# Performance work log

Hardware: AMD Instinct MI355X
Metric: run time of the kernel (lower is better)

The kernel has to match this reference:

```python
import jax, jax.numpy as jnp
import numpy as np

N, H, W, C = 128, 256, 256, 3
P = 1.0
XFLIP = 1.0
YFLIP = 1.0
ROTATE_INT = 1.0
TRANSLATE_INT = 1.0
TRANSLATE_INT_MAX = 0.125


def setup_inputs() -> dict:
    key = jax.random.key(0)
    ks = jax.random.split(key, 9)
    return {
        'images': jax.random.normal(ks[0], (N, H, W, C), dtype=jnp.float32),
        'xflip_w': jax.random.randint(ks[1], (N, 1, 1, 1), 0, 2, dtype=jnp.int32),
        'xflip_gate': jax.random.uniform(ks[2], (N, 1, 1, 1), dtype=jnp.float32),
        'yflip_w': jax.random.randint(ks[3], (N, 1, 1, 1), 0, 2, dtype=jnp.int32),
        'yflip_gate': jax.random.uniform(ks[4], (N, 1, 1, 1), dtype=jnp.float32),
        'rot_w': jax.random.randint(ks[5], (N, 1, 1, 1), 0, 4, dtype=jnp.int32),
        'rot_gate': jax.random.uniform(ks[6], (N, 1, 1, 1), dtype=jnp.float32),
        'trans_w': jax.random.uniform(ks[7], (2, N, 1, 1, 1), dtype=jnp.float32),
        'trans_gate': jax.random.uniform(ks[8], (1, N, 1, 1, 1), dtype=jnp.float32),
    }


def _augment(images, xflip_w, xflip_gate, yflip_w, yflip_gate, rot_w, rot_gate,
             trans_w, trans_gate):
    n, h, w_, c = images.shape

    # --- x-flip (per-sample gated horizontal flip) ---
    wv = jnp.where(xflip_gate < XFLIP * P, xflip_w, jnp.zeros_like(xflip_w))
    images = jnp.where(wv == 1, jnp.flip(images, 2), images)

    # --- y-flip ---
    wv = jnp.where(yflip_gate < YFLIP * P, yflip_w, jnp.zeros_like(yflip_w))
    images = jnp.where(wv == 1, jnp.flip(images, 1), images)

    # --- 90-degree rotations (requires H == W) ---
    wv = jnp.where(rot_gate < ROTATE_INT * P, rot_w, jnp.zeros_like(rot_w))
    images = jnp.where((wv == 1) | (wv == 2), jnp.flip(images, 2), images)
    images = jnp.where((wv == 2) | (wv == 3), jnp.flip(images, 1), images)
    images = jnp.where((wv == 1) | (wv == 3), jnp.transpose(images, (0, 2, 1, 3)), images)

    # --- integer translation with reflection padding (gather) ---
    tw = trans_w * 2.0 - 1.0                                   # [2,N,1,1,1] in [-1,1)
    tw = jnp.where(trans_gate < TRANSLATE_INT * P, tw, jnp.zeros_like(tw))
    tx = jnp.round(tw[0] * w_ * TRANSLATE_INT_MAX).astype(jnp.int32)[:, 0, 0, 0]  # [N]
    ty = jnp.round(tw[1] * h * TRANSLATE_INT_MAX).astype(jnp.int32)[:, 0, 0, 0]   # [N]
    tx = jax.lax.stop_gradient(tx)
    ty = jax.lax.stop_gradient(ty)
    # reflected source indices per sample: [N, W] and [N, H]
    xi = w_ - 1 - jnp.abs(w_ - 1 - (jnp.arange(w_)[None, :] - tx[:, None]) % (w_ * 2 - 2))
    yi = h - 1 - jnp.abs(h - 1 - (jnp.arange(h)[None, :] + ty[:, None]) % (h * 2 - 2))
    images = jax.vmap(lambda im, y, x: im[y][:, x])(images, yi, xi)
    return images


def reference(images, xflip_w, xflip_gate, yflip_w, yflip_gate, rot_w, rot_gate,
              trans_w, trans_gate):
    return _augment(images, xflip_w, xflip_gate, yflip_w, yflip_gate,
                    rot_w, rot_gate, trans_w, trans_gate)
```

## Files before the change

### kernel.cpp

```cpp
#include <hip/hip_runtime.h>

#define NN 128
#define HH 256
#define WW 256
#define CC 3
#define HWC (HH * WW * CC)
#define TILE 32
#define LSTRIDE 100
#define ROWF (WW * CC)

__device__ __forceinline__ int reflect_idx(int v, int size) {
    int period = 2 * size - 2;
    int m = v % period;
    if (m < 0) m += period;
    return size - 1 - abs(size - 1 - m);
}

__global__ __launch_bounds__(256) void augment_kernel(
    const float* __restrict__ images,
    const int*   __restrict__ xflip_w,
    const float* __restrict__ xflip_gate,
    const int*   __restrict__ yflip_w,
    const float* __restrict__ yflip_gate,
    const int*   __restrict__ rot_w,
    const float* __restrict__ rot_gate,
    const float* __restrict__ trans_w,
    const float* __restrict__ trans_gate,
    float* __restrict__ out)
{
    __shared__ __align__(16) int   syv768[TILE];
    __shared__ __align__(16) int   sxc[96];
    __shared__ __align__(16) int   taddr[96];
    __shared__ __align__(16) float tile[TILE * LSTRIDE];

    const int n       = blockIdx.x >> 6;
    const int tile_id = blockIdx.x & 63;
    const int yo0     = (tile_id >> 3) << 5;
    const int xo0     = (tile_id & 7) << 5;

    const bool xf = (xflip_gate[n] < 1.0f) && (xflip_w[n] == 1);
    const bool yf = (yflip_gate[n] < 1.0f) && (yflip_w[n] == 1);
    const int  rw = (rot_gate[n] < 1.0f) ? rot_w[n] : 0;
    const bool fx = ((rw == 1) || (rw == 2)) ^ xf;
    const bool fy = ((rw == 2) || (rw == 3)) ^ yf;
    const bool tr = (rw == 1) || (rw == 3);

    float tw0 = trans_w[n]      * 2.0f - 1.0f;
    float tw1 = trans_w[NN + n] * 2.0f - 1.0f;
    if (!(trans_gate[n] < 1.0f)) { tw0 = 0.0f; tw1 = 0.0f; }
    const int tx = (int)rintf(tw0 * (WW * 0.125f));
    const int ty = (int)rintf(tw1 * (HH * 0.125f));

    {
        const int t = threadIdx.x;
        if (t < TILE) {
            int v = tr ? reflect_idx(xo0 + t - tx, WW)
                       : reflect_idx(yo0 + t + ty, HH);
            if (fy) v = HH - 1 - v;
            syv768[t] = v * ROWF;
        } else if (t < 64) {
            const int u = t - 32;
            int v = tr ? reflect_idx(yo0 + u + ty, HH)
                       : reflect_idx(xo0 + u - tx, WW);
            if (fx) v = WW - 1 - v;
            taddr[u] = v;
        }
    }
    __syncthreads();
    {
        const int t = threadIdx.x;
        if (t < 96) {
            const int j = t / 3, c = t - j * 3;
            sxc[t] = taddr[j] * 3 + c;
        }
    }
    __syncthreads();
    {
        const int t = threadIdx.x;
        if (t < 96) {
            const int j = t / 3, c = t - j * 3;
            taddr[t] = j * LSTRIDE + c;
        }
    }
    __syncthreads();

    const float* __restrict__ src = images + (size_t)n * HWC;
    const size_t outBase = (size_t)(n * HH + yo0) * ROWF + xo0 * CC;
    float4* __restrict__ out4 = (float4*)(out + outBase);
    const int4* sxc4 = (const int4*)sxc;
    const int4* ta4  = (const int4*)taddr;

    if (!tr) {
        int   ib[3], qb[3];
        int4  off[3];
        float vals[12];
        #pragma unroll
        for (int v = 0; v < 3; ++v) {
            const int f = v * 256 + threadIdx.x;
            ib[v] = f / 24;
            qb[v] = f - ib[v] * 24;
            off[v] = sxc4[qb[v]];
        }
        #pragma unroll
        for (int v = 0; v < 3; ++v) {
            const int base = syv768[ib[v]];
            vals[v * 4 + 0] = src[base + off[v].x];
            vals[v * 4 + 1] = src[base + off[v].y];
            vals[v * 4 + 2] = src[base + off[v].z];
            vals[v * 4 + 3] = src[base + off[v].w];
        }
        #pragma unroll
        for (int v = 0; v < 3; ++v) {
            out4[ib[v] * (ROWF / 4) + qb[v]] =
                make_float4(vals[v * 4 + 0], vals[v * 4 + 1],
                            vals[v * 4 + 2], vals[v * 4 + 3]);
        }
    } else {
        int   jb[3], qb[3];
        int4  off[3], tof[3];
        float vals[12];
        #pragma unroll
        for (int v = 0; v < 3; ++v) {
            const int f = v * 256 + threadIdx.x;
            jb[v] = f / 24;
            qb[v] = f - jb[v] * 24;
            off[v] = sxc4[qb[v]];
            tof[v] = ta4[qb[v]];
        }
        #pragma unroll
        for (int v = 0; v < 3; ++v) {
            const int base = syv768[jb[v]];
            vals[v * 4 + 0] = src[base + off[v].x];
            vals[v * 4 + 1] = src[base + off[v].y];
            vals[v * 4 + 2] = src[base + off[v].z];
            vals[v * 4 + 3] = src[base + off[v].w];
        }
        #pragma unroll
        for (int v = 0; v < 3; ++v) {
            const int jc = jb[v] * 3;
            tile[tof[v].x + jc] = vals[v * 4 + 0];
            tile[tof[v].y + jc] = vals[v * 4 + 1];
            tile[tof[v].z + jc] = vals[v * 4 + 2];
            tile[tof[v].w + jc] = vals[v * 4 + 3];
        }
        __syncthreads();
        const float4* tile4 = (const float4*)tile;
        #pragma unroll
        for (int v = 0; v < 3; ++v) {
            const int f = v * 256 + threadIdx.x;
            const int i = f / 24;
            const int q = f - i * 24;
            out4[i * (ROWF / 4) + q] = tile4[i * (LSTRIDE / 4) + q];
        }
    }
}

extern "C" void kernel_launch(void* const* d_in, const int* in_sizes, int n_in,
                              void* d_out, int out_size, void* d_ws, size_t ws_size,
                              hipStream_t stream)
{
    const float* images     = (const float*)d_in[0];
    const int*   xflip_w    = (const int*)  d_in[1];
    const float* xflip_gate = (const float*)d_in[2];
    const int*   yflip_w    = (const int*)  d_in[3];
    const float* yflip_gate = (const float*)d_in[4];
    const int*   rot_w      = (const int*)  d_in[5];
    const float* rot_gate   = (const float*)d_in[6];
    const float* trans_w    = (const float*)d_in[7];
    const float* trans_gate = (const float*)d_in[8];
    float* outp = (float*)d_out;

    dim3 grid(NN * 64);
    dim3 block(256);
    augment_kernel<<<grid, block, 0, stream>>>(images, xflip_w, xflip_gate,
                                               yflip_w, yflip_gate, rot_w, rot_gate,
                                               trans_w, trans_gate, outp);
}
```

Measured before the change: 38.11 us.

## Remap block order, merge index setup, use scalar transpose path with odd LDS stride

Block IDs are permuted so that consecutive blocks come from different images and tile groups, which spreads memory traffic. The source-index setup is collapsed from three barrier-separated phases into one. The transposed path now uses scalar loads, LDS writes and stores over a tile with odd stride 99 in place of float4 vectors with stride 100, aiming to reduce LDS bank conflicts. The cost is more scalar memory instructions and extra index arithmetic per element.

```diff
diff --git a/kernel.cpp b/kernel.cpp
--- a/kernel.cpp
+++ b/kernel.cpp
@@ -5,9 +5,8 @@
 #define WW 256
 #define CC 3
 #define HWC (HH * WW * CC)
-#define TILE 32
-#define LSTRIDE 100
 #define ROWF (WW * CC)
+#define LSTR 99
 
 __device__ __forceinline__ int reflect_idx(int v, int size) {
     int period = 2 * size - 2;
@@ -28,13 +27,14 @@
     const float* __restrict__ trans_gate,
     float* __restrict__ out)
 {
-    __shared__ __align__(16) int   syv768[TILE];
+    __shared__ __align__(16) int   syv768[32];
     __shared__ __align__(16) int   sxc[96];
-    __shared__ __align__(16) int   taddr[96];
-    __shared__ __align__(16) float tile[TILE * LSTRIDE];
+    __shared__ __align__(16) float tile[32 * LSTR];
 
-    const int n       = blockIdx.x >> 6;
-    const int tile_id = blockIdx.x & 63;
+    const int bid     = blockIdx.x;
+    const int logical = (bid & 7) * 1024 + (bid >> 3);
+    const int n       = logical >> 6;
+    const int tile_id = logical & 63;
     const int yo0     = (tile_id >> 3) << 5;
     const int xo0     = (tile_id & 7) << 5;
 
@@ -53,44 +53,30 @@
 
     {
         const int t = threadIdx.x;
-        if (t < TILE) {
-            int v = tr ? reflect_idx(xo0 + t - tx, WW)
-                       : reflect_idx(yo0 + t + ty, HH);
+        if (t < 96) {
+            const int b = (t * 171) >> 9;
+            const int c = t - 3 * b;
+            int v = tr ? reflect_idx(yo0 + b + ty, HH)
+                       : reflect_idx(xo0 + b - tx, WW);
+            if (fx) v = WW - 1 - v;
+            sxc[t] = v * 3 + c;
+        } else if (t < 128) {
+            const int a = t - 96;
+            int v = tr ? reflect_idx(xo0 + a - tx, WW)
+                       : reflect_idx(yo0 + a + ty, HH);
             if (fy) v = HH - 1 - v;
-            syv768[t] = v * ROWF;
-        } else if (t < 64) {
-            const int u = t - 32;
-            int v = tr ? reflect_idx(yo0 + u + ty, HH)
-                       : reflect_idx(xo0 + u - tx, WW);
-            if (fx) v = WW - 1 - v;
-            taddr[u] = v;
-        }
-    }
-    __syncthreads();
-    {
-        const int t = threadIdx.x;
-        if (t < 96) {
-            const int j = t / 3, c = t - j * 3;
-            sxc[t] = taddr[j] * 3 + c;
-        }
-    }
-    __syncthreads();
-    {
-        const int t = threadIdx.x;
-        if (t < 96) {
-            const int j = t / 3, c = t - j * 3;
-            taddr[t] = j * LSTRIDE + c;
+            syv768[a] = v * ROWF;
         }
     }
     __syncthreads();
 
     const float* __restrict__ src = images + (size_t)n * HWC;
-    const size_t outBase = (size_t)(n * HH + yo0) * ROWF + xo0 * CC;
-    float4* __restrict__ out4 = (float4*)(out + outBase);
-    const int4* sxc4 = (const int4*)sxc;
-    const int4* ta4  = (const int4*)taddr;
 
     if (!tr) {
+        const size_t outBase = (size_t)(n * HH + yo0) * ROWF + xo0 * CC;
+        float4* __restrict__ out4 = (float4*)(out + outBase);
+        const int4* sxc4 = (const int4*)sxc;
+
         int   ib[3], qb[3];
         int4  off[3];
         float vals[12];
@@ -116,41 +102,34 @@
                             vals[v * 4 + 2], vals[v * 4 + 3]);
         }
     } else {
-        int   jb[3], qb[3];
-        int4  off[3], tof[3];
         float vals[12];
         #pragma unroll
-        for (int v = 0; v < 3; ++v) {
-            const int f = v * 256 + threadIdx.x;
-            jb[v] = f / 24;
-            qb[v] = f - jb[v] * 24;
-            off[v] = sxc4[qb[v]];
-            tof[v] = ta4[qb[v]];
+        for (int v = 0; v < 12; ++v) {
+            const int f  = threadIdx.x + v * 256;
+            const int g  = f >> 5;
+            const int j  = (g * 171) >> 9;
+            const int m  = f - 96 * j;
+            vals[v] = src[syv768[j] + sxc[m]];
         }
         #pragma unroll
-        for (int v = 0; v < 3; ++v) {
-            const int base = syv768[jb[v]];
-            vals[v * 4 + 0] = src[base + off[v].x];
-            vals[v * 4 + 1] = src[base + off[v].y];
-            vals[v * 4 + 2] = src[base + off[v].z];
-            vals[v * 4 + 3] = src[base + off[v].w];
-        }
-        #pragma unroll
-        for (int v = 0; v < 3; ++v) {
-            const int jc = jb[v] * 3;
-            tile[tof[v].x + jc] = vals[v * 4 + 0];
-            tile[tof[v].y + jc] = vals[v * 4 + 1];
-            tile[tof[v].z + jc] = vals[v * 4 + 2];
-            tile[tof[v].w + jc] = vals[v * 4 + 3];
+        for (int v = 0; v < 12; ++v) {
+            const int f  = threadIdx.x + v * 256;
+            const int g  = f >> 5;
+            const int j  = (g * 171) >> 9;
+            const int m  = f - 96 * j;
+            const int i  = (m * 171) >> 9;
+            const int c  = m - 3 * i;
+            tile[i * LSTR + 3 * j + c] = vals[v];
         }
         __syncthreads();
-        const float4* tile4 = (const float4*)tile;
+        const size_t outB = (size_t)(n * HH + yo0) * ROWF + xo0 * CC;
         #pragma unroll
-        for (int v = 0; v < 3; ++v) {
-            const int f = v * 256 + threadIdx.x;
-            const int i = f / 24;
-            const int q = f - i * 24;
-            out4[i * (ROWF / 4) + q] = tile4[i * (LSTRIDE / 4) + q];
+        for (int v = 0; v < 12; ++v) {
+            const int e = threadIdx.x + v * 256;
+            const int g = e >> 5;
+            const int i = (g * 171) >> 9;
+            const int k = e - 96 * i;
+            out[outB + (size_t)i * ROWF + k] = tile[i * LSTR + k];
         }
     }
 }
```

Measured after the change: 34.62 us. 1.1x faster.
